# Optimization experiments

Hardware: AMD Instinct MI355X
Metric: run time of the kernel (lower is better)

Reference implementation:

```python
import jax, jax.numpy as jnp
import numpy as np

N, F, C, H, HX = 100000, 500, 40, 256, 64
E = 1_600_000


def setup_inputs() -> dict:
    key = jax.random.key(0)
    ks = jax.random.split(key, 12)
    s = lambda fan_in: 1.0 / np.sqrt(fan_in)
    return {
        "x": jax.random.normal(ks[0], (N, F), dtype=jnp.float32),
        "y": jax.random.randint(ks[1], (N,), 0, C),
        "train_mask": jax.random.randint(ks[2], (N,), 0, 2).astype(bool),
        "edge_index": jax.random.randint(ks[3], (2, E), 0, N),
        "edge_index_neg": jax.random.randint(ks[4], (2, E), 0, N),
        "fc1_w": jax.random.uniform(ks[5], (H, F), jnp.float32, -s(F), s(F)),
        "fc1_b": jnp.zeros((H,), jnp.float32),
        "fc2_w": jax.random.uniform(ks[6], (C, H), jnp.float32, -s(H), s(H)),
        "fc2_b": jnp.zeros((C,), jnp.float32),
        "xenc_w": jax.random.uniform(ks[7], (HX, F), jnp.float32, -s(F), s(F)),
        "xenc_b": jnp.zeros((HX,), jnp.float32),
        "pexy_w": jax.random.uniform(ks[8], (1, 2 * (HX + C)), jnp.float32, -s(2 * (HX + C)), s(2 * (HX + C))),
        "pexy_b": jnp.zeros((1,), jnp.float32),
    }


def reference(x, y, train_mask, edge_index, edge_index_neg,
              fc1_w, fc1_b, fc2_w, fc2_b, xenc_w, xenc_b, pexy_w, pexy_b):
    temperature = 1.0
    # MLP p(y|x), inference mode (dropout is identity)
    h = jax.nn.relu(x @ fc1_w.T + fc1_b)
    logits = (h @ fc2_w.T + fc2_b) / temperature
    y_log_prob = jax.nn.log_softmax(logits, axis=-1)            # [N, C]
    y_prob = jnp.exp(y_log_prob)
    one_hot = jax.nn.one_hot(y, y_prob.shape[1], dtype=y_prob.dtype)
    y_prob = jnp.where(train_mask[:, None], one_hot, y_prob)    # [N, C]

    # node encoder
    xe = jax.nn.relu(x @ xenc_w.T + xenc_b)                     # [N, HX]

    # The scorer Linear(2*(HX+C) -> 1) applied to cat([x_q, x_k, y_q, y_k])
    # decomposes into per-node query/key scalars (same math, no big concat):
    hx = xe.shape[1]
    w = pexy_w[0]
    w_xq, w_xk = w[:hx], w[hx:2 * hx]
    w_yq, w_yk = w[2 * hx:2 * hx + y_prob.shape[1]], w[2 * hx + y_prob.shape[1]:]
    s_q = xe @ w_xq + y_prob @ w_yq                             # [N]
    s_k = xe @ w_xk + y_prob @ w_yk                             # [N]

    def edge_scores(ei):
        return (s_q[ei[0]] + s_k[ei[1]] + pexy_b[0])[:, None]   # [E, 1]

    e_pred_pos = edge_scores(edge_index)
    e_pred_neg = edge_scores(edge_index_neg)
    return (e_pred_pos, e_pred_neg, y_log_prob)
```

## Files before the change

kernel.cpp:

```cpp
#include <hip/hip_runtime.h>
#include <stdint.h>

#define N_NODES 100000
#define F_DIM   500
#define C_DIM   40
#define H_DIM   256
#define HX_DIM  64
#define O_DIM   320
#define E_NUM   1600000

typedef unsigned short u16;
typedef unsigned int   u32;
typedef __attribute__((ext_vector_type(4))) u16    u16x4;
typedef __attribute__((ext_vector_type(8))) u16    u16x8;
typedef __attribute__((ext_vector_type(4))) float  f32x4;
typedef __attribute__((ext_vector_type(8))) short  bf16x8;

__device__ __forceinline__ float bf2f(u16 v) {
  u32 u = ((u32)v) << 16;
  return __builtin_bit_cast(float, u);
}
__device__ __forceinline__ u16 f2bf(float f) {
  u32 x = __builtin_bit_cast(u32, f);
  x += 0x7fffu + ((x >> 16) & 1u);
  return (u16)(x >> 16);
}

__global__ __launch_bounds__(256) void k_detect(const u32* __restrict__ tm, int* __restrict__ flag)
{
  __shared__ int s;
  if (threadIdx.x == 0) s = 0;
  __syncthreads();
  int local = 0;
  #pragma unroll
  for (int j = 0; j < 16; ++j) {
    if (tm[j * 256 + threadIdx.x] > 1u) local = 1;
  }
  if (local) s = 1;
  __syncthreads();
  if (threadIdx.x == 0) *flag = s;
}

__global__ __launch_bounds__(256) void k_cvtw(
    const float* __restrict__ fc1w, const float* __restrict__ xencw, u16* __restrict__ wws)
{
  const int g = blockIdx.x * 256 + threadIdx.x;
  const int c = g / 1280;
  const int rem = g - c * 1280;
  const int r = rem >> 2;
  const int k0 = c * 32 + (rem & 3) * 8;
  const float* src = (r < H_DIM) ? (fc1w + (long)r * F_DIM)
                                 : (xencw + (long)(r - H_DIM) * F_DIM);
  f32x4 v0 = {0.f, 0.f, 0.f, 0.f}, v1 = v0;
  if (k0 + 4 <= F_DIM) v0 = *(const f32x4*)(src + k0);
  if (k0 + 8 <= F_DIM) v1 = *(const f32x4*)(src + k0 + 4);
  u16x8 o;
  #pragma unroll
  for (int i = 0; i < 4; ++i) { o[i] = f2bf(v0[i]); o[4 + i] = f2bf(v1[i]); }
  *(u16x8*)(wws + (size_t)g * 8) = o;
}

#define G_BM 64
#define G_BK 32
#define BN   320
#define RH_LD 328

__global__ __launch_bounds__(512, 4) void k_fused(
    const float* __restrict__ x, const u16* __restrict__ wws,
    const float* __restrict__ fc1b, const float* __restrict__ xencb,
    const int* __restrict__ y, const void* __restrict__ tmask,
    const float* __restrict__ fc2w, const float* __restrict__ fc2b,
    const float* __restrict__ pw, const int* __restrict__ mask_flag,
    float* __restrict__ out_lp, float* __restrict__ sq_out, float* __restrict__ sk_out)
{
  __shared__ __align__(16) u16 smem[36736];
  u16* sAl  = smem;
  u16* sOut = smem;
  u16* sBp  = smem + 20992;

  const int tid  = threadIdx.x;
  const int lane = tid & 63;
  const int wid  = tid >> 6;
  const int wr   = wid >> 2;
  const int wcol = wid & 3;
  const int l15 = lane & 15, lgrp = lane >> 4;
  const long rowbase = (long)blockIdx.x * G_BM;

  const int ar   = tid >> 3;
  const int as   = tid & 7;
  const int glog = as >> 1, half = as & 1;
  const int gph  = glog ^ ((ar >> 1) & 3);
  const long arow = rowbase + ar;
  const bool arv = (arow < N_NODES);
  const float* xrow = x + arow * F_DIM;
  const int rslot = (lgrp ^ ((l15 >> 1) & 3)) * 8;

  const u16* bbase = wws + (wcol * 80 + l15) * 32 + lgrp * 8;

#define LOAD_B(dst, kc)                                                        \
  {                                                                            \
    const u16* bp = bbase + (size_t)(kc) * (BN * G_BK);                        \
    _Pragma("unroll")                                                          \
    for (int n = 0; n < 5; ++n) dst[n] = *(const bf16x8*)(bp + n * 512);       \
  }

  bf16x8 bX[5], bY[5], bZ[5];
  LOAD_B(bX, 0);
  LOAD_B(bY, 1);

  f32x4 xr[8];
  #pragma unroll
  for (int c = 0; c < 8; ++c) {
    xr[c] = (f32x4){0.f, 0.f, 0.f, 0.f};
    if (arv) xr[c] = *(const f32x4*)(xrow + c * 32 + as * 4);
  }
  #pragma unroll
  for (int c = 0; c < 8; ++c) {
    u16x4 o;
    #pragma unroll
    for (int i = 0; i < 4; ++i) o[i] = f2bf(xr[c][i]);
    *(u16x4*)(sAl + c * 2048 + ar * 32 + gph * 8 + half * 4) = o;
  }
  #pragma unroll
  for (int c = 8; c < 16; ++c) {
    const int k0 = c * 32 + as * 4;
    xr[c - 8] = (f32x4){0.f, 0.f, 0.f, 0.f};
    if (arv && k0 + 4 <= F_DIM) xr[c - 8] = *(const f32x4*)(xrow + k0);
  }
  #pragma unroll
  for (int c = 8; c < 16; ++c) {
    u16x4 o;
    #pragma unroll
    for (int i = 0; i < 4; ++i) o[i] = f2bf(xr[c - 8][i]);
    *(u16x4*)(sAl + c * 2048 + ar * 32 + gph * 8 + half * 4) = o;
  }

  f32x4 acc[2][5];
  #pragma unroll
  for (int m = 0; m < 2; ++m)
    #pragma unroll
    for (int n = 0; n < 5; ++n)
      acc[m][n] = (f32x4){0.f, 0.f, 0.f, 0.f};

  __syncthreads();

#define GS(kc, BU, BL)                                                         \
  {                                                                            \
    if ((kc) + 2 < 16) LOAD_B(BL, (kc) + 2);                                   \
    const u16* sa = sAl + (kc) * 2048 + (wr * 32 + l15) * 32 + rslot;          \
    _Pragma("unroll")                                                          \
    for (int m = 0; m < 2; ++m) {                                              \
      const bf16x8 afr = *(const bf16x8*)(sa + m * 512);                       \
      _Pragma("unroll")                                                        \
      for (int n = 0; n < 5; ++n)                                              \
        acc[m][n] = __builtin_amdgcn_mfma_f32_16x16x32_bf16(afr, BU[n], acc[m][n], 0, 0, 0); \
    }                                                                          \
  }

  GS(0,  bX, bZ)  GS(1,  bY, bX)  GS(2,  bZ, bY)  GS(3,  bX, bZ)
  GS(4,  bY, bX)  GS(5,  bZ, bY)  GS(6,  bX, bZ)  GS(7,  bY, bX)
  GS(8,  bZ, bY)  GS(9,  bX, bZ)  GS(10, bY, bX)  GS(11, bZ, bY)
  GS(12, bX, bZ)  GS(13, bY, bX)  GS(14, bZ, bY)  GS(15, bX, bY)

  __syncthreads();

  #pragma unroll
  for (int n = 0; n < 5; ++n) {
    const int col = wcol * 80 + n * 16 + l15;
    const float bias = (col < H_DIM) ? fc1b[col] : xencb[col - H_DIM];
    #pragma unroll
    for (int m = 0; m < 2; ++m) {
      const int r0 = wr * 32 + m * 16 + lgrp * 4;
      #pragma unroll
      for (int rg = 0; rg < 4; ++rg)
        sOut[(r0 + rg) * RH_LD + col] = f2bf(fmaxf(acc[m][n][rg] + bias, 0.f));
    }
  }
  #pragma unroll
  for (int it = 0; it < 4; ++it) {
    const int g = it * 512 + tid;
    if (g < 1920) {
      const int r = g / 40, c = g - r * 40;
      const int k0 = c * 8;
      u16x8 v = {0, 0, 0, 0, 0, 0, 0, 0};
      const float* src = nullptr;
      if (r < C_DIM) { if (k0 < H_DIM) src = fc2w + r * H_DIM + k0; }
      else if (r == C_DIM)     { if (k0 >= H_DIM) src = pw + (k0 - H_DIM); }
      else if (r == C_DIM + 1) { if (k0 >= H_DIM) src = pw + HX_DIM + (k0 - H_DIM); }
      if (src) {
        const f32x4 v0 = *(const f32x4*)src;
        const f32x4 v1 = *(const f32x4*)(src + 4);
        #pragma unroll
        for (int i = 0; i < 4; ++i) { v[i] = f2bf(v0[i]); v[4 + i] = f2bf(v1[i]); }
      }
      *(u16x8*)&sBp[r * RH_LD + c * 8] = v;
    }
  }
  __syncthreads();

  if (wid < 4) {
    f32x4 racc[3];
    #pragma unroll
    for (int n = 0; n < 3; ++n) racc[n] = (f32x4){0.f, 0.f, 0.f, 0.f};
    const u16* pa = &sOut[(wid * 16 + l15) * RH_LD + lgrp * 8];
    const u16* pb = &sBp[l15 * RH_LD + lgrp * 8];
    #pragma unroll
    for (int kc = 0; kc < 10; ++kc) {
      const bf16x8 a = *(const bf16x8*)(pa + kc * 32);
      #pragma unroll
      for (int n = 0; n < 3; ++n) {
        const bf16x8 b = *(const bf16x8*)(pb + n * 16 * RH_LD + kc * 32);
        racc[n] = __builtin_amdgcn_mfma_f32_16x16x32_bf16(a, b, racc[n], 0, 0, 0);
      }
    }

    const int c0 = l15, c1 = 16 + l15, c2 = 32 + l15;
    const bool v2 = (l15 < 8);
    const float b0 = fc2b[c0], b1 = fc2b[c1], b2 = v2 ? fc2b[c2] : 0.f;
    const float wq0 = pw[2 * HX_DIM + c0], wq1 = pw[2 * HX_DIM + c1],
                wq2 = v2 ? pw[2 * HX_DIM + c2] : 0.f;
    const float wk0 = pw[2 * HX_DIM + C_DIM + c0], wk1 = pw[2 * HX_DIM + C_DIM + c1],
                wk2 = v2 ? pw[2 * HX_DIM + C_DIM + c2] : 0.f;
    const bool byte_mask = (*mask_flag != 0);

    #pragma unroll
    for (int rg = 0; rg < 4; ++rg) {
      const long row = rowbase + wid * 16 + lgrp * 4 + rg;
      const bool rv = (row < N_NODES);
      const long rowc = rv ? row : (N_NODES - 1);
      const float lg0 = racc[0][rg] + b0;
      const float lg1 = racc[1][rg] + b1;
      const float lg2 = racc[2][rg] + b2;
      const float sxq = __shfl(racc[2][rg], (lane & 48) | 8, 64);
      const float sxk = __shfl(racc[2][rg], (lane & 48) | 9, 64);

      float m = fmaxf(lg0, lg1);
      if (v2) m = fmaxf(m, lg2);
      #pragma unroll
      for (int off = 1; off < 16; off <<= 1) m = fmaxf(m, __shfl_xor(m, off, 64));
      const float e0 = __expf(lg0 - m), e1 = __expf(lg1 - m),
                  e2 = v2 ? __expf(lg2 - m) : 0.f;
      float s = e0 + e1 + e2;
      #pragma unroll
      for (int off = 1; off < 16; off <<= 1) s += __shfl_xor(s, off, 64);
      const float lse = m + __logf(s);
      const float inv = 1.f / s;

      const int yv = y[rowc];
      const bool tm = byte_mask ? (((const unsigned char*)tmask)[rowc] != 0)
                                : (((const int*)tmask)[rowc] != 0);
      const float p0 = tm ? (c0 == yv ? 1.f : 0.f) : e0 * inv;
      const float p1 = tm ? (c1 == yv ? 1.f : 0.f) : e1 * inv;
      const float p2 = tm ? (c2 == yv ? 1.f : 0.f) : e2 * inv;
      float sq = p0 * wq0 + p1 * wq1 + p2 * wq2;
      float sk = p0 * wk0 + p1 * wk1 + p2 * wk2;
      #pragma unroll
      for (int off = 1; off < 16; off <<= 1) {
        sq += __shfl_xor(sq, off, 64);
        sk += __shfl_xor(sk, off, 64);
      }

      if (rv) {
        float* lp = out_lp + row * C_DIM;
        lp[c0] = lg0 - lse;
        lp[c1] = lg1 - lse;
        if (v2) lp[c2] = lg2 - lse;
        if (l15 == 0) { sq_out[row] = sq + sxq; sk_out[row] = sk + sxk; }
      }
    }
  }
#undef LOAD_B
#undef GS
}

__global__ __launch_bounds__(256) void k_edges(
    const int* __restrict__ ei, const int* __restrict__ ein,
    const float* __restrict__ sq, const float* __restrict__ sk,
    const float* __restrict__ pb, float* __restrict__ out)
{
  const int e = blockIdx.x * 256 + threadIdx.x;
  if (e >= E_NUM) return;
  const float b = pb[0];
  const int a0 = ei[e],  a1 = ei[E_NUM + e];
  out[e] = sq[a0] + sk[a1] + b;
  const int c0 = ein[e], c1 = ein[E_NUM + e];
  out[E_NUM + e] = sq[c0] + sk[c1] + b;
}

extern "C" void kernel_launch(void* const* d_in, const int* in_sizes, int n_in,
                              void* d_out, int out_size, void* d_ws, size_t ws_size,
                              hipStream_t stream)
{
  const float* x     = (const float*)d_in[0];
  const int*   y     = (const int*)d_in[1];
  const void*  tm    = d_in[2];
  const int*   ei    = (const int*)d_in[3];
  const int*   ein   = (const int*)d_in[4];
  const float* fc1w  = (const float*)d_in[5];
  const float* fc1b  = (const float*)d_in[6];
  const float* fc2w  = (const float*)d_in[7];
  const float* fc2b  = (const float*)d_in[8];
  const float* xencw = (const float*)d_in[9];
  const float* xencb = (const float*)d_in[10];
  const float* pw    = (const float*)d_in[11];
  const float* pb    = (const float*)d_in[12];
  float* out = (float*)d_out;

  float* sq   = (float*)((char*)d_ws + (size_t)N_NODES * O_DIM * 2);
  float* sk   = sq + N_NODES;
  int*   flag = (int*)(sk + N_NODES);
  u16*   wws  = (u16*)((char*)d_ws + 64800064);

  k_detect<<<1, 256, 0, stream>>>((const u32*)tm, flag);
  k_cvtw  <<<80, 256, 0, stream>>>(fc1w, xencw, wws);
  const int nrb = (N_NODES + G_BM - 1) / G_BM;
  k_fused <<<nrb, 512, 0, stream>>>(x, wws, fc1b, xencb, y, tm, fc2w, fc2b, pw, flag,
                                    out + 2 * (size_t)E_NUM, sq, sk);
  k_edges <<<E_NUM / 256, 256, 0, stream>>>(ei, ein, sq, sk, pb, out);
}
```

Baseline: 140.5 us.

## Load GEMM A fragments straight from global memory instead of staging through LDS

The fused MLP/encoder GEMM no longer stages the block's x tile into shared memory as bf16. Each wave now loads its own fp32 A-fragment rows from global memory, converts them to bf16 in registers, and feeds the MFMAs, prefetching the next k-step's A and B. This drops the LDS store/load round trip and the two block-wide barriers around it, and cuts B buffering from triple to double. In exchange, every x row is fetched separately by the four column waves, the per-lane 32-byte global reads are less coalesced, and out-of-range rows and k indices are clamped, which relies on zero-padded weights.

```diff
diff --git a/kernel.cpp b/kernel.cpp
--- a/kernel.cpp
+++ b/kernel.cpp
@@ -74,7 +74,6 @@
     float* __restrict__ out_lp, float* __restrict__ sq_out, float* __restrict__ sk_out)
 {
   __shared__ __align__(16) u16 smem[36736];
-  u16* sAl  = smem;
   u16* sOut = smem;
   u16* sBp  = smem + 20992;
 
@@ -86,83 +85,62 @@
   const int l15 = lane & 15, lgrp = lane >> 4;
   const long rowbase = (long)blockIdx.x * G_BM;
 
-  const int ar   = tid >> 3;
-  const int as   = tid & 7;
-  const int glog = as >> 1, half = as & 1;
-  const int gph  = glog ^ ((ar >> 1) & 3);
-  const long arow = rowbase + ar;
-  const bool arv = (arow < N_NODES);
-  const float* xrow = x + arow * F_DIM;
-  const int rslot = (lgrp ^ ((l15 >> 1) & 3)) * 8;
+  long r0 = rowbase + wr * 32 + l15;
+  long r1 = r0 + 16;
+  if (r0 > N_NODES - 1) r0 = N_NODES - 1;
+  if (r1 > N_NODES - 1) r1 = N_NODES - 1;
+  const float* ap0 = x + r0 * F_DIM;
+  const float* ap1 = x + r1 * F_DIM;
 
   const u16* bbase = wws + (wcol * 80 + l15) * 32 + lgrp * 8;
 
-#define LOAD_B(dst, kc)                                                        \
+  f32x4 acc[2][5];
+  #pragma unroll
+  for (int m = 0; m < 2; ++m)
+    #pragma unroll
+    for (int n = 0; n < 5; ++n)
+      acc[m][n] = (f32x4){0.f, 0.f, 0.f, 0.f};
+
+  f32x4 a0l, a0h, a1l, a1h;
+  bf16x8 bP[5], bQ[5];
+
+#define LA(kc)                                                                 \
+  {                                                                            \
+    const int k0 = (kc) * G_BK + lgrp * 8;                                     \
+    const int ka = (k0     > 496) ? 496 : k0;                                  \
+    const int kb = (k0 + 4 > 496) ? 496 : (k0 + 4);                            \
+    a0l = *(const f32x4*)(ap0 + ka);  a0h = *(const f32x4*)(ap0 + kb);         \
+    a1l = *(const f32x4*)(ap1 + ka);  a1h = *(const f32x4*)(ap1 + kb);         \
+  }
+
+#define LB(dst, kc)                                                            \
   {                                                                            \
     const u16* bp = bbase + (size_t)(kc) * (BN * G_BK);                        \
     _Pragma("unroll")                                                          \
     for (int n = 0; n < 5; ++n) dst[n] = *(const bf16x8*)(bp + n * 512);       \
   }
 
-  bf16x8 bX[5], bY[5], bZ[5];
-  LOAD_B(bX, 0);
-  LOAD_B(bY, 1);
-
-  f32x4 xr[8];
-  #pragma unroll
-  for (int c = 0; c < 8; ++c) {
-    xr[c] = (f32x4){0.f, 0.f, 0.f, 0.f};
-    if (arv) xr[c] = *(const f32x4*)(xrow + c * 32 + as * 4);
-  }
-  #pragma unroll
-  for (int c = 0; c < 8; ++c) {
-    u16x4 o;
-    #pragma unroll
-    for (int i = 0; i < 4; ++i) o[i] = f2bf(xr[c][i]);
-    *(u16x4*)(sAl + c * 2048 + ar * 32 + gph * 8 + half * 4) = o;
-  }
-  #pragma unroll
-  for (int c = 8; c < 16; ++c) {
-    const int k0 = c * 32 + as * 4;
-    xr[c - 8] = (f32x4){0.f, 0.f, 0.f, 0.f};
-    if (arv && k0 + 4 <= F_DIM) xr[c - 8] = *(const f32x4*)(xrow + k0);
-  }
-  #pragma unroll
-  for (int c = 8; c < 16; ++c) {
-    u16x4 o;
-    #pragma unroll
-    for (int i = 0; i < 4; ++i) o[i] = f2bf(xr[c - 8][i]);
-    *(u16x4*)(sAl + c * 2048 + ar * 32 + gph * 8 + half * 4) = o;
-  }
-
-  f32x4 acc[2][5];
-  #pragma unroll
-  for (int m = 0; m < 2; ++m)
-    #pragma unroll
-    for (int n = 0; n < 5; ++n)
-      acc[m][n] = (f32x4){0.f, 0.f, 0.f, 0.f};
-
-  __syncthreads();
-
 #define GS(kc, BU, BL)                                                         \
   {                                                                            \
-    if ((kc) + 2 < 16) LOAD_B(BL, (kc) + 2);                                   \
-    const u16* sa = sAl + (kc) * 2048 + (wr * 32 + l15) * 32 + rslot;          \
+    bf16x8 af0, af1;                                                           \
     _Pragma("unroll")                                                          \
-    for (int m = 0; m < 2; ++m) {                                              \
-      const bf16x8 afr = *(const bf16x8*)(sa + m * 512);                       \
-      _Pragma("unroll")                                                        \
-      for (int n = 0; n < 5; ++n)                                              \
-        acc[m][n] = __builtin_amdgcn_mfma_f32_16x16x32_bf16(afr, BU[n], acc[m][n], 0, 0, 0); \
+    for (int i = 0; i < 4; ++i) {                                              \
+      af0[i]     = (short)f2bf(a0l[i]);  af0[4 + i] = (short)f2bf(a0h[i]);     \
+      af1[i]     = (short)f2bf(a1l[i]);  af1[4 + i] = (short)f2bf(a1h[i]);     \
     }                                                                          \
-  }
-
-  GS(0,  bX, bZ)  GS(1,  bY, bX)  GS(2,  bZ, bY)  GS(3,  bX, bZ)
-  GS(4,  bY, bX)  GS(5,  bZ, bY)  GS(6,  bX, bZ)  GS(7,  bY, bX)
-  GS(8,  bZ, bY)  GS(9,  bX, bZ)  GS(10, bY, bX)  GS(11, bZ, bY)
-  GS(12, bX, bZ)  GS(13, bY, bX)  GS(14, bZ, bY)  GS(15, bX, bY)
-
-  __syncthreads();
+    if ((kc) < 15) { LA((kc) + 1); LB(BL, (kc) + 1); }                         \
+    _Pragma("unroll")                                                          \
+    for (int n = 0; n < 5; ++n) {                                              \
+      acc[0][n] = __builtin_amdgcn_mfma_f32_16x16x32_bf16(af0, BU[n], acc[0][n], 0, 0, 0); \
+      acc[1][n] = __builtin_amdgcn_mfma_f32_16x16x32_bf16(af1, BU[n], acc[1][n], 0, 0, 0); \
+    }                                                                          \
+  }
+
+  LA(0); LB(bP, 0);
+  GS(0,  bP, bQ)  GS(1,  bQ, bP)  GS(2,  bP, bQ)  GS(3,  bQ, bP)
+  GS(4,  bP, bQ)  GS(5,  bQ, bP)  GS(6,  bP, bQ)  GS(7,  bQ, bP)
+  GS(8,  bP, bQ)  GS(9,  bQ, bP)  GS(10, bP, bQ)  GS(11, bQ, bP)
+  GS(12, bP, bQ)  GS(13, bQ, bP)  GS(14, bP, bQ)  GS(15, bQ, bP)
 
   #pragma unroll
   for (int n = 0; n < 5; ++n) {
@@ -170,10 +148,10 @@
     const float bias = (col < H_DIM) ? fc1b[col] : xencb[col - H_DIM];
     #pragma unroll
     for (int m = 0; m < 2; ++m) {
-      const int r0 = wr * 32 + m * 16 + lgrp * 4;
+      const int rr0 = wr * 32 + m * 16 + lgrp * 4;
       #pragma unroll
       for (int rg = 0; rg < 4; ++rg)
-        sOut[(r0 + rg) * RH_LD + col] = f2bf(fmaxf(acc[m][n][rg] + bias, 0.f));
+        sOut[(rr0 + rg) * RH_LD + col] = f2bf(fmaxf(acc[m][n][rg] + bias, 0.f));
     }
   }
   #pragma unroll
@@ -269,7 +247,8 @@
       }
     }
   }
-#undef LOAD_B
+#undef LA
+#undef LB
 #undef GS
 }
 
```

New measurement: 163.7 us. 1.17x slower.
